# Kernel optimization log

Measured on AMD Instinct MI355X. Metric: run time of the kernel, lower is better.

Reference implementation:

```python
import jax, jax.numpy as jnp
import numpy as np

D_K = 64
N_HEADS = 12
LN_EPS = 1e-5


def layer_norm(x, eps=LN_EPS):
    # nn.LayerNorm(768) is created fresh each forward -> weight=1, bias=0
    mu = jnp.mean(x, axis=-1, keepdims=True)
    var = jnp.mean(jnp.square(x - mu), axis=-1, keepdims=True)
    return (x - mu) * jax.lax.rsqrt(var + eps)


def setup_inputs() -> dict:
    key = jax.random.key(0)
    ks = jax.random.split(key, 7)
    B, S, D = 2, 2048, 768
    scale = 1.0 / np.sqrt(D)
    return {
        "input_Q": jax.random.normal(ks[0], (B, S, D), jnp.float32),
        "input_K": jax.random.normal(ks[1], (B, S, D), jnp.float32),
        "input_V": jax.random.normal(ks[2], (B, S, D), jnp.float32),
        "Wq": jax.random.normal(ks[3], (D, D), jnp.float32) * scale,
        "Wk": jax.random.normal(ks[4], (D, D), jnp.float32) * scale,
        "Wv": jax.random.normal(ks[5], (D, D), jnp.float32) * scale,
        "Wo": jax.random.normal(ks[6], (D, D), jnp.float32) * scale,
    }


def reference(input_Q, input_K, input_V, Wq, Wk, Wv, Wo):
    B, Sq, D = input_Q.shape
    Sk = input_K.shape[1]
    H, dk = N_HEADS, D_K
    residual = input_Q
    # projections: [B,S,D] @ [D, H*dk] -> [B,H,S,dk]
    Q = (input_Q @ Wq).reshape(B, Sq, H, dk).transpose(0, 2, 1, 3)
    K = (input_K @ Wk).reshape(B, Sk, H, dk).transpose(0, 2, 1, 3)
    V = (input_V @ Wv).reshape(B, Sk, H, dk).transpose(0, 2, 1, 3)
    # attention scores [B,H,Sq,Sk]
    att = jnp.einsum("bhqd,bhkd->bhqk", Q, K) / np.sqrt(dk).astype(np.float32)
    att = jax.nn.softmax(att, axis=-1)
    ctx = jnp.einsum("bhqk,bhkd->bhqd", att, V)  # [B,H,Sq,dk]
    ctx = ctx.transpose(0, 2, 1, 3).reshape(B, Sq, H * dk)
    out = ctx @ Wo
    return layer_norm(out + residual)
```

## Files before the change

### kernel.cpp

```cpp
#include <hip/hip_runtime.h>
#include <hip/hip_bf16.h>
#include <stdint.h>

#define S_LEN 2048
#define D_MODEL 768
#define NH 12
#define DK 64
#define BATCH 2
#define M_TOT (BATCH * S_LEN)

typedef __attribute__((ext_vector_type(8))) short short8;
typedef __attribute__((ext_vector_type(4))) float f32x4;
typedef __attribute__((ext_vector_type(16))) float f32x16;

__device__ inline short f2bf(float f) {
  union { float f; uint32_t u; } v; v.f = f;
  uint32_t r = v.u + 0x7fffu + ((v.u >> 16) & 1u);
  return (short)(r >> 16);
}

__device__ inline f32x4 mfma16(short8 a, short8 b, f32x4 c) {
  return __builtin_amdgcn_mfma_f32_16x16x32_bf16(a, b, c, 0, 0, 0);
}
__device__ inline f32x16 mfma32(short8 a, short8 b, f32x16 c) {
  return __builtin_amdgcn_mfma_f32_32x32x16_bf16(a, b, c, 0, 0, 0);
}

__device__ inline void gl16(const void* g, void* l) {
  __builtin_amdgcn_global_load_lds(
      (const __attribute__((address_space(1))) unsigned*)g,
      (__attribute__((address_space(3))) unsigned*)l, 16, 0, 0);
}

__device__ inline unsigned cvtpk(float lo, float hi) {
  unsigned r;
  asm("v_cvt_pk_bf16_f32 %0, %1, %2" : "=v"(r) : "v"(lo), "v"(hi));
  return r;
}
__device__ inline void plswap(unsigned& a, unsigned& b) {
  asm("v_permlane32_swap_b32 %0, %1" : "+v"(a), "+v"(b));
}
__device__ inline float lo16(uint32_t u) {
  union { uint32_t u; float f; } x; x.u = u << 16; return x.f;
}
__device__ inline float hi16(uint32_t u) {
  union { uint32_t u; float f; } x; x.u = u & 0xffff0000u; return x.f;
}

__global__ __launch_bounds__(256) void transpose_w_kernel(
    const float* __restrict__ Wq, const float* __restrict__ Wk,
    const float* __restrict__ Wv, const float* __restrict__ Wo,
    short* __restrict__ WT) {
  int z = blockIdx.z;
  const float* W = z == 0 ? Wq : (z == 1 ? Wk : (z == 2 ? Wv : Wo));
  short* O = WT + (size_t)z * D_MODEL * D_MODEL;
  __shared__ float t[32][33];
  int x = threadIdx.x, y = threadIdx.y;
  int nb = blockIdx.x * 32, kb = blockIdx.y * 32;
#pragma unroll
  for (int j = 0; j < 4; ++j)
    t[y + 8 * j][x] = W[(kb + y + 8 * j) * D_MODEL + nb + x];
  __syncthreads();
#pragma unroll
  for (int j = 0; j < 4; ++j)
    O[(nb + y + 8 * j) * D_MODEL + kb + x] = f2bf(t[x][y + 8 * j]);
}

__global__ __launch_bounds__(256) void cast_x_kernel(
    const float* __restrict__ Xq, const float* __restrict__ Xk,
    const float* __restrict__ Xv, short* __restrict__ Xb) {
  int z = blockIdx.y;
  const float* X = z == 0 ? Xq : (z == 1 ? Xk : Xv);
  short* O = Xb + (size_t)z * M_TOT * D_MODEL;
  size_t i = ((size_t)blockIdx.x * 256 + threadIdx.x) * 8;
  float4 f0 = *(const float4*)(X + i);
  float4 f1 = *(const float4*)(X + i + 4);
  short8 v;
  v[0] = f2bf(f0.x); v[1] = f2bf(f0.y); v[2] = f2bf(f0.z); v[3] = f2bf(f0.w);
  v[4] = f2bf(f1.x); v[5] = f2bf(f1.y); v[6] = f2bf(f1.z); v[7] = f2bf(f1.w);
  *(short8*)(O + i) = v;
}

__global__ __launch_bounds__(256) void proj_kernel(
    const short* __restrict__ Xb, const short* __restrict__ WTall,
    short* __restrict__ Qo, short* __restrict__ Ko, short* __restrict__ Vo) {
  int bid = blockIdx.x;
  int wk = (bid & 7) * 72 + (bid >> 3);
  int which = wk / 192;
  int rem = wk % 192;
  int mt = rem / 6, nt = rem % 6;
  int mbase = mt * 128, nbase = nt * 128;
  const short* X = Xb + (size_t)which * M_TOT * D_MODEL;
  const short* WT = WTall + (size_t)which * D_MODEL * D_MODEL;

  __shared__ short As[128][32];
  __shared__ short Bs[128][32];
  int tid = threadIdx.x;
  int wv = tid >> 6, lane = tid & 63, r = lane & 15, g = lane >> 4;
  int wm = (wv & 1) * 64, wn = (wv >> 1) * 64;
  int srow = (lane >> 2), scol = (lane & 3) * 8;

  f32x4 acc[4][4] = {};
  for (int kk = 0; kk < D_MODEL; kk += 32) {
#pragma unroll
    for (int j = 0; j < 2; ++j) {
      int row = wv * 32 + j * 16;
      gl16(X + (size_t)(mbase + row + srow) * D_MODEL + kk + scol, &As[row][0]);
      gl16(WT + (size_t)(nbase + row + srow) * D_MODEL + kk + scol, &Bs[row][0]);
    }
    __syncthreads();
    short8 a[4], b[4];
#pragma unroll
    for (int i = 0; i < 4; ++i) {
      a[i] = *(short8*)&As[wm + i * 16 + r][g * 8];
      b[i] = *(short8*)&Bs[wn + i * 16 + r][g * 8];
    }
#pragma unroll
    for (int i = 0; i < 4; ++i)
#pragma unroll
      for (int j = 0; j < 4; ++j)
        acc[i][j] = mfma16(a[i], b[j], acc[i][j]);
    __syncthreads();
  }
#pragma unroll
  for (int i = 0; i < 4; ++i)
#pragma unroll
    for (int j = 0; j < 4; ++j)
#pragma unroll
      for (int reg = 0; reg < 4; ++reg) {
        int m = mbase + wm + i * 16 + g * 4 + reg;
        int n = nbase + wn + j * 16 + r;
        int b_ = m >> 11, s = m & 2047, h = n >> 6, d = n & 63;
        if (which == 0) {
          short v = f2bf(acc[i][j][reg] * 0.18033688f);
          Qo[(((size_t)b_ * NH + h) * S_LEN + s) * DK + d] = v;
        } else if (which == 1) {
          short v = f2bf(acc[i][j][reg]);
          Ko[(((size_t)b_ * NH + h) * S_LEN + s) * DK + (d ^ ((s & 7) << 3))] = v;
        } else {
          short v = f2bf(acc[i][j][reg]);
          Vo[(((size_t)b_ * NH + h) * DK + d) * S_LEN + (s ^ ((d & 7) << 3))] = v;
        }
      }
}

__global__ __launch_bounds__(256) void attn_kernel(
    const short* __restrict__ Qg, const short* __restrict__ Kg,
    const short* __restrict__ Vt, short* __restrict__ oP,
    float* __restrict__ mlP) {
  int bh = blockIdx.y;
  int split = blockIdx.z;
  int tid = threadIdx.x;
  int w = tid >> 6, lane = tid & 63;
  int c32 = lane & 31, hi = lane >> 5;
  int qbase = blockIdx.x * 128 + w * 32;
  int kc0 = split * (S_LEN / 2);
  const short* qp = Qg + (size_t)bh * S_LEN * DK;
  const char* kp = (const char*)(Kg + (size_t)bh * S_LEN * DK);
  const char* vp = (const char*)(Vt + (size_t)bh * DK * S_LEN);

  short8 qf[4];
#pragma unroll
  for (int kk = 0; kk < 4; ++kk)
    qf[kk] = *(const short8*)(qp + (size_t)(qbase + c32) * DK + kk * 16 + hi * 8);

  f32x16 o0 = {}, o1 = {};
  float m_run = -30000.f, l_run = 0.f;
  const int NT = (S_LEN / 2) / 64;
  int sw = (c32 & 7) << 4;

  for (int t = 0; t < NT; ++t) {
    int kc = kc0 + t * 64;
    const char* kt = kp + (size_t)kc * 128;
    const char* vt = vp + (size_t)kc * 2;

    f32x16 st0 = {}, st1 = {};
#pragma unroll
    for (int kk = 0; kk < 4; ++kk) {
      int cb = kk * 32 + hi * 16;
      short8 k0 = *(const short8*)(kt + (size_t)c32 * 128 + (cb ^ sw));
      short8 k1 = *(const short8*)(kt + (size_t)(32 + c32) * 128 + (cb ^ sw));
      st0 = mfma32(k0, qf[kk], st0);
      st1 = mfma32(k1, qf[kk], st1);
    }

    short8 vl0[4], vl1[4];
#pragma unroll
    for (int ks = 0; ks < 4; ++ks) {
      int cb = ks * 32 + hi * 16;
      vl0[ks] = *(const short8*)(vt + (size_t)c32 * 4096 + (cb ^ sw));
      vl1[ks] = *(const short8*)(vt + (size_t)(32 + c32) * 4096 + (cb ^ sw));
    }

    float cm = -30000.f;
#pragma unroll
    for (int i = 0; i < 16; ++i) cm = fmaxf(cm, fmaxf(st0[i], st1[i]));
    cm = fmaxf(cm, __shfl_xor(cm, 32));
    if (!__all(cm <= m_run + 8.0f)) {
      float m_new = fmaxf(m_run, cm);
      float al = __builtin_amdgcn_exp2f(m_run - m_new);
      l_run *= al;
      m_run = m_new;
#pragma unroll
      for (int r = 0; r < 16; ++r) {
        int ql = (r & 3) + 8 * (r >> 2) + 4 * hi;
        float ar = __shfl(al, ql);
        o0[r] *= ar;
        o1[r] *= ar;
      }
    }
    float csum = 0.f;
#pragma unroll
    for (int i = 0; i < 16; ++i) {
      st0[i] = __builtin_amdgcn_exp2f(st0[i] - m_run);
      st1[i] = __builtin_amdgcn_exp2f(st1[i] - m_run);
      csum += st0[i] + st1[i];
    }
    csum += __shfl_xor(csum, 32);
    l_run += csum;

#pragma unroll
    for (int ks = 0; ks < 4; ++ks) {
      f32x16 P = (ks < 2) ? st0 : st1;
      int s8 = (ks & 1) * 8;
      unsigned A = cvtpk(P[s8 + 0], P[s8 + 1]);
      unsigned Bx = cvtpk(P[s8 + 4], P[s8 + 5]);
      unsigned C = cvtpk(P[s8 + 2], P[s8 + 3]);
      unsigned Dx = cvtpk(P[s8 + 6], P[s8 + 7]);
      plswap(A, Bx);
      plswap(C, Dx);
      union { unsigned u[4]; short8 s; } pu;
      pu.u[0] = A; pu.u[1] = C; pu.u[2] = Bx; pu.u[3] = Dx;
      o0 = mfma32(pu.s, vl0[ks], o0);
      o1 = mfma32(pu.s, vl1[ks], o1);
    }
  }

  size_t pbase = ((size_t)split * 24 + bh) * S_LEN;
#pragma unroll
  for (int r = 0; r < 16; ++r) {
    int ql = (r & 3) + 8 * (r >> 2) + 4 * hi;
    float linv = 1.0f / __shfl(l_run, ql);
    short* op = oP + (pbase + qbase + ql) * DK;
    op[c32] = f2bf(o0[r] * linv);
    op[32 + c32] = f2bf(o1[r] * linv);
  }
  if (hi == 0) {
    float* mlp = mlP + (pbase + qbase + c32) * 2;
    mlp[0] = m_run;
    mlp[1] = l_run;
  }
}

__global__ __launch_bounds__(256) void merge_kernel(
    const short* __restrict__ oP, const float* __restrict__ mlP,
    short* __restrict__ Cx) {
  int t = blockIdx.x * 256 + threadIdx.x;
  int q = t >> 5, dp = (t & 31) * 2;
  const int NQ = 24 * S_LEN;
  float2 ml0 = *(const float2*)(mlP + (size_t)q * 2);
  float2 ml1 = *(const float2*)(mlP + ((size_t)NQ + q) * 2);
  float m = fmaxf(ml0.x, ml1.x);
  float a0 = ml0.y * __builtin_amdgcn_exp2f(ml0.x - m);
  float a1 = ml1.y * __builtin_amdgcn_exp2f(ml1.x - m);
  float inv = 1.0f / (a0 + a1);
  float w0 = a0 * inv, w1 = a1 * inv;
  uint32_t a = *(const uint32_t*)(oP + (size_t)q * DK + dp);
  uint32_t b2 = *(const uint32_t*)(oP + ((size_t)NQ + q) * DK + dp);
  float v0 = lo16(a) * w0 + lo16(b2) * w1;
  float v1 = hi16(a) * w0 + hi16(b2) * w1;
  int bh = q >> 11, sr = q & 2047, b = bh / NH, h = bh % NH;
  uint32_t outw = (uint32_t)(uint16_t)f2bf(v0) | ((uint32_t)(uint16_t)f2bf(v1) << 16);
  *(uint32_t*)(Cx + ((size_t)(b * S_LEN + sr)) * D_MODEL + h * DK + dp) = outw;
}

__global__ __launch_bounds__(256) void gemm_out_kernel(
    const short* __restrict__ ctx, const short* __restrict__ WoT,
    const float* __restrict__ resid, float* __restrict__ Y) {
  int bid = blockIdx.x;
  int wk = (bid & 7) * 24 + (bid >> 3);
  int mt = wk / 6, nt = wk % 6;
  int mbase = mt * 128, nbase = nt * 128;

  __shared__ short As[128][32];
  __shared__ short Bs[128][32];
  int tid = threadIdx.x;
  int wv = tid >> 6, lane = tid & 63, r = lane & 15, g = lane >> 4;
  int wm = (wv & 1) * 64, wn = (wv >> 1) * 64;
  int srow = (lane >> 2), scol = (lane & 3) * 8;

  f32x4 acc[4][4] = {};
  for (int kk = 0; kk < D_MODEL; kk += 32) {
#pragma unroll
    for (int j = 0; j < 2; ++j) {
      int row = wv * 32 + j * 16;
      gl16(ctx + (size_t)(mbase + row + srow) * D_MODEL + kk + scol, &As[row][0]);
      gl16(WoT + (size_t)(nbase + row + srow) * D_MODEL + kk + scol, &Bs[row][0]);
    }
    __syncthreads();
    short8 a[4], b[4];
#pragma unroll
    for (int i = 0; i < 4; ++i) {
      a[i] = *(short8*)&As[wm + i * 16 + r][g * 8];
      b[i] = *(short8*)&Bs[wn + i * 16 + r][g * 8];
    }
#pragma unroll
    for (int i = 0; i < 4; ++i)
#pragma unroll
      for (int j = 0; j < 4; ++j)
        acc[i][j] = mfma16(a[i], b[j], acc[i][j]);
    __syncthreads();
  }
#pragma unroll
  for (int i = 0; i < 4; ++i)
#pragma unroll
    for (int j = 0; j < 4; ++j)
#pragma unroll
      for (int reg = 0; reg < 4; ++reg) {
        int m = mbase + wm + i * 16 + g * 4 + reg;
        int n = nbase + wn + j * 16 + r;
        Y[(size_t)m * D_MODEL + n] = acc[i][j][reg] + resid[(size_t)m * D_MODEL + n];
      }
}

__global__ __launch_bounds__(256) void ln_kernel(const float* __restrict__ Y,
                                                 float* __restrict__ out) {
  int row = blockIdx.x * 4 + (threadIdx.x >> 6);
  int l = threadIdx.x & 63;
  const float* yp = Y + (size_t)row * D_MODEL;
  float v[12];
  float s = 0.f, q = 0.f;
#pragma unroll
  for (int c = 0; c < 12; ++c) {
    v[c] = yp[c * 64 + l];
    s += v[c];
    q += v[c] * v[c];
  }
#pragma unroll
  for (int d = 1; d < 64; d <<= 1) {
    s += __shfl_xor(s, d);
    q += __shfl_xor(q, d);
  }
  float mu = s * (1.0f / 768.0f);
  float var = q * (1.0f / 768.0f) - mu * mu;
  float rstd = rsqrtf(var + 1e-5f);
  float* op = out + (size_t)row * D_MODEL;
#pragma unroll
  for (int c = 0; c < 12; ++c)
    op[c * 64 + l] = (v[c] - mu) * rstd;
}

extern "C" void kernel_launch(void* const* d_in, const int* in_sizes, int n_in,
                              void* d_out, int out_size, void* d_ws, size_t ws_size,
                              hipStream_t stream) {
  const float* xq = (const float*)d_in[0];
  const float* xk = (const float*)d_in[1];
  const float* xv = (const float*)d_in[2];
  const float* Wq = (const float*)d_in[3];
  const float* Wk = (const float*)d_in[4];
  const float* Wv = (const float*)d_in[5];
  const float* Wo = (const float*)d_in[6];
  float* out = (float*)d_out;

  char* ws = (char*)d_ws;
  const size_t WSZ = (size_t)D_MODEL * D_MODEL;
  const size_t QSZ = (size_t)M_TOT * D_MODEL;
  short* WT = (short*)ws;
  short* Xb = WT + 4 * WSZ;
  short* Qb = Xb + 3 * QSZ;
  short* Kb = Qb + QSZ;
  short* Vb = Kb + QSZ;
  short* Cx = Vb + QSZ;
  short* oP = Xb;
  float* mlP = (float*)(Xb + (size_t)2 * 24 * S_LEN * DK);
  float* Yf = (float*)Xb;

  transpose_w_kernel<<<dim3(24, 24, 4), dim3(32, 8), 0, stream>>>(Wq, Wk, Wv, Wo, WT);
  cast_x_kernel<<<dim3(1536, 3), 256, 0, stream>>>(xq, xk, xv, Xb);
  proj_kernel<<<576, 256, 0, stream>>>(Xb, WT, Qb, Kb, Vb);
  attn_kernel<<<dim3(16, 24, 2), 256, 0, stream>>>(Qb, Kb, Vb, oP, mlP);
  merge_kernel<<<6144, 256, 0, stream>>>(oP, mlP, Cx);
  gemm_out_kernel<<<192, 256, 0, stream>>>(Cx, WT + 3 * WSZ, xq, Yf);
  ln_kernel<<<1024, 256, 0, stream>>>(Yf, out);
}
```

Measured before the change: 223.7 us.

## Double-buffer GEMM LDS tiles and register-prefetch K tiles in attention

The projection and output GEMMs now use two LDS buffers, issuing the next k-slice's global-to-LDS loads before computing on the current one. They wait with explicit vmcnt counts and raw s_barrier instead of __syncthreads. In attention, the next K tile is prefetched into registers while the current one feeds the score MFMAs, and the V loads are hoisted ahead of the score compute. This is meant to hide global memory latency behind MFMA work, at the cost of doubled LDS, more registers and reliance on hand-counted waitcnt correctness.

```diff
diff --git a/kernel.cpp b/kernel.cpp
--- a/kernel.cpp
+++ b/kernel.cpp
@@ -93,35 +93,49 @@
   const short* X = Xb + (size_t)which * M_TOT * D_MODEL;
   const short* WT = WTall + (size_t)which * D_MODEL * D_MODEL;
 
-  __shared__ short As[128][32];
-  __shared__ short Bs[128][32];
+  __shared__ short As[2][128][32];
+  __shared__ short Bs[2][128][32];
   int tid = threadIdx.x;
   int wv = tid >> 6, lane = tid & 63, r = lane & 15, g = lane >> 4;
   int wm = (wv & 1) * 64, wn = (wv >> 1) * 64;
   int srow = (lane >> 2), scol = (lane & 3) * 8;
 
+#define PSTAGE(buf, kk)                                                        \
+  {                                                                            \
+    _Pragma("unroll") for (int j = 0; j < 2; ++j) {                            \
+      int row = wv * 32 + j * 16;                                              \
+      gl16(X + (size_t)(mbase + row + srow) * D_MODEL + (kk) + scol,           \
+           &As[buf][row][0]);                                                  \
+      gl16(WT + (size_t)(nbase + row + srow) * D_MODEL + (kk) + scol,          \
+           &Bs[buf][row][0]);                                                  \
+    }                                                                          \
+  }
+
   f32x4 acc[4][4] = {};
-  for (int kk = 0; kk < D_MODEL; kk += 32) {
-#pragma unroll
-    for (int j = 0; j < 2; ++j) {
-      int row = wv * 32 + j * 16;
-      gl16(X + (size_t)(mbase + row + srow) * D_MODEL + kk + scol, &As[row][0]);
-      gl16(WT + (size_t)(nbase + row + srow) * D_MODEL + kk + scol, &Bs[row][0]);
-    }
-    __syncthreads();
+  PSTAGE(0, 0);
+  for (int kt = 0; kt < 24; ++kt) {
+    int cur = kt & 1;
+    if (kt < 23) {
+      PSTAGE(cur ^ 1, (kt + 1) * 32);
+      asm volatile("s_waitcnt vmcnt(4)" ::: "memory");
+    } else {
+      asm volatile("s_waitcnt vmcnt(0)" ::: "memory");
+    }
+    __builtin_amdgcn_s_barrier();
     short8 a[4], b[4];
 #pragma unroll
     for (int i = 0; i < 4; ++i) {
-      a[i] = *(short8*)&As[wm + i * 16 + r][g * 8];
-      b[i] = *(short8*)&Bs[wn + i * 16 + r][g * 8];
+      a[i] = *(short8*)&As[cur][wm + i * 16 + r][g * 8];
+      b[i] = *(short8*)&Bs[cur][wn + i * 16 + r][g * 8];
     }
 #pragma unroll
     for (int i = 0; i < 4; ++i)
 #pragma unroll
       for (int j = 0; j < 4; ++j)
         acc[i][j] = mfma16(a[i], b[j], acc[i][j]);
-    __syncthreads();
-  }
+    __builtin_amdgcn_s_barrier();
+  }
+#undef PSTAGE
 #pragma unroll
   for (int i = 0; i < 4; ++i)
 #pragma unroll
@@ -164,32 +178,57 @@
   for (int kk = 0; kk < 4; ++kk)
     qf[kk] = *(const short8*)(qp + (size_t)(qbase + c32) * DK + kk * 16 + hi * 8);
 
+  int sw = (c32 & 7) << 4;
+  int ko0[4], ko1[4], vo0[4], vo1[4];
+#pragma unroll
+  for (int i = 0; i < 4; ++i) {
+    int cb = i * 32 + hi * 16;
+    ko0[i] = c32 * 128 + (cb ^ sw);
+    ko1[i] = (32 + c32) * 128 + (cb ^ sw);
+    vo0[i] = c32 * 4096 + (cb ^ sw);
+    vo1[i] = (32 + c32) * 4096 + (cb ^ sw);
+  }
+
+  short8 kr0[4], kr1[4];
+  {
+    const char* kt0 = kp + (size_t)kc0 * 128;
+#pragma unroll
+    for (int i = 0; i < 4; ++i) {
+      kr0[i] = *(const short8*)(kt0 + ko0[i]);
+      kr1[i] = *(const short8*)(kt0 + ko1[i]);
+    }
+  }
+
   f32x16 o0 = {}, o1 = {};
   float m_run = -30000.f, l_run = 0.f;
   const int NT = (S_LEN / 2) / 64;
-  int sw = (c32 & 7) << 4;
 
   for (int t = 0; t < NT; ++t) {
     int kc = kc0 + t * 64;
-    const char* kt = kp + (size_t)kc * 128;
     const char* vt = vp + (size_t)kc * 2;
 
+    short8 vl0[4], vl1[4];
+#pragma unroll
+    for (int ks = 0; ks < 4; ++ks) {
+      vl0[ks] = *(const short8*)(vt + vo0[ks]);
+      vl1[ks] = *(const short8*)(vt + vo1[ks]);
+    }
+
     f32x16 st0 = {}, st1 = {};
 #pragma unroll
     for (int kk = 0; kk < 4; ++kk) {
-      int cb = kk * 32 + hi * 16;
-      short8 k0 = *(const short8*)(kt + (size_t)c32 * 128 + (cb ^ sw));
-      short8 k1 = *(const short8*)(kt + (size_t)(32 + c32) * 128 + (cb ^ sw));
-      st0 = mfma32(k0, qf[kk], st0);
-      st1 = mfma32(k1, qf[kk], st1);
-    }
-
-    short8 vl0[4], vl1[4];
-#pragma unroll
-    for (int ks = 0; ks < 4; ++ks) {
-      int cb = ks * 32 + hi * 16;
-      vl0[ks] = *(const short8*)(vt + (size_t)c32 * 4096 + (cb ^ sw));
-      vl1[ks] = *(const short8*)(vt + (size_t)(32 + c32) * 4096 + (cb ^ sw));
+      st0 = mfma32(kr0[kk], qf[kk], st0);
+      st1 = mfma32(kr1[kk], qf[kk], st1);
+    }
+
+    {
+      int tn = (t + 1 < NT) ? t + 1 : NT - 1;
+      const char* ktn = kp + (size_t)(kc0 + tn * 64) * 128;
+#pragma unroll
+      for (int i = 0; i < 4; ++i) {
+        kr0[i] = *(const short8*)(ktn + ko0[i]);
+        kr1[i] = *(const short8*)(ktn + ko1[i]);
+      }
     }
 
     float cm = -30000.f;
@@ -282,35 +321,49 @@
   int mt = wk / 6, nt = wk % 6;
   int mbase = mt * 128, nbase = nt * 128;
 
-  __shared__ short As[128][32];
-  __shared__ short Bs[128][32];
+  __shared__ short As[2][128][32];
+  __shared__ short Bs[2][128][32];
   int tid = threadIdx.x;
   int wv = tid >> 6, lane = tid & 63, r = lane & 15, g = lane >> 4;
   int wm = (wv & 1) * 64, wn = (wv >> 1) * 64;
   int srow = (lane >> 2), scol = (lane & 3) * 8;
 
+#define GSTAGE(buf, kk)                                                        \
+  {                                                                            \
+    _Pragma("unroll") for (int j = 0; j < 2; ++j) {                            \
+      int row = wv * 32 + j * 16;                                              \
+      gl16(ctx + (size_t)(mbase + row + srow) * D_MODEL + (kk) + scol,         \
+           &As[buf][row][0]);                                                  \
+      gl16(WoT + (size_t)(nbase + row + srow) * D_MODEL + (kk) + scol,         \
+           &Bs[buf][row][0]);                                                  \
+    }                                                                          \
+  }
+
   f32x4 acc[4][4] = {};
-  for (int kk = 0; kk < D_MODEL; kk += 32) {
-#pragma unroll
-    for (int j = 0; j < 2; ++j) {
-      int row = wv * 32 + j * 16;
-      gl16(ctx + (size_t)(mbase + row + srow) * D_MODEL + kk + scol, &As[row][0]);
-      gl16(WoT + (size_t)(nbase + row + srow) * D_MODEL + kk + scol, &Bs[row][0]);
-    }
-    __syncthreads();
+  GSTAGE(0, 0);
+  for (int kt = 0; kt < 24; ++kt) {
+    int cur = kt & 1;
+    if (kt < 23) {
+      GSTAGE(cur ^ 1, (kt + 1) * 32);
+      asm volatile("s_waitcnt vmcnt(4)" ::: "memory");
+    } else {
+      asm volatile("s_waitcnt vmcnt(0)" ::: "memory");
+    }
+    __builtin_amdgcn_s_barrier();
     short8 a[4], b[4];
 #pragma unroll
     for (int i = 0; i < 4; ++i) {
-      a[i] = *(short8*)&As[wm + i * 16 + r][g * 8];
-      b[i] = *(short8*)&Bs[wn + i * 16 + r][g * 8];
+      a[i] = *(short8*)&As[cur][wm + i * 16 + r][g * 8];
+      b[i] = *(short8*)&Bs[cur][wn + i * 16 + r][g * 8];
     }
 #pragma unroll
     for (int i = 0; i < 4; ++i)
 #pragma unroll
       for (int j = 0; j < 4; ++j)
         acc[i][j] = mfma16(a[i], b[j], acc[i][j]);
-    __syncthreads();
-  }
+    __builtin_amdgcn_s_barrier();
+  }
+#undef GSTAGE
 #pragma unroll
   for (int i = 0; i < 4; ++i)
 #pragma unroll
```

Result: faster. 219.0 us (-2.1%).
